# Kernel tuning notes

Hardware: AMD Instinct MI355X
Metric: run time of the kernel (lower is better)

Reference implementation:

```python
import jax, jax.numpy as jnp
import numpy as np

T, HID, H, KV, D = 2048, 2048, 16, 8, 128
EPS = 1e-6
THETA = 10000.0


def setup_inputs() -> dict:
    key = jax.random.key(0)
    ks = jax.random.split(key, 4)
    return {
        "positions": jnp.arange(T, dtype=jnp.int32),
        "hidden_states": jax.random.normal(ks[0], (T, HID), dtype=jnp.float32),
        "layernorm_weight": jnp.ones((HID,), dtype=jnp.float32),
        "qkv_weight": jax.random.normal(ks[1], ((H + 2 * KV) * D, HID), dtype=jnp.float32) * 0.02,
        "q_norm_weight": jnp.ones((D,), dtype=jnp.float32),
        "k_norm_weight": jnp.ones((D,), dtype=jnp.float32),
        "o_weight": jax.random.normal(ks[2], (HID, H * D), dtype=jnp.float32) * 0.02,
    }


def _rms(x, w, eps=EPS):
    var = jnp.mean(jnp.square(x), axis=-1, keepdims=True)
    return x * jax.lax.rsqrt(var + eps) * w


def _rope(x, pos):
    # NeoX-style rotary over full head_dim. x: [T, nH, D]
    inv_freq = 1.0 / (THETA ** (jnp.arange(0, D, 2, dtype=jnp.float32) / D))
    ang = pos.astype(jnp.float32)[:, None] * inv_freq  # [T, D/2]
    cos, sin = jnp.cos(ang)[:, None, :], jnp.sin(ang)[:, None, :]
    x1, x2 = x[..., : D // 2], x[..., D // 2 :]
    return jnp.concatenate([x1 * cos - x2 * sin, x2 * cos + x1 * sin], axis=-1)


def reference(positions, hidden_states, layernorm_weight, qkv_weight,
              q_norm_weight, k_norm_weight, o_weight):
    # Fused RMSNorm + QKV projection
    normed = _rms(hidden_states, layernorm_weight)                 # [T, HID]
    qkv = normed @ qkv_weight.T                                    # [T, (H+2KV)*D]
    q, k, v = jnp.split(qkv, [H * D, (H + KV) * D], axis=-1)
    q = _rms(q.reshape(T, H, D), q_norm_weight)                    # per-head q norm
    k = _rms(k.reshape(T, KV, D), k_norm_weight)                   # per-head k norm
    v = v.reshape(T, KV, D)
    # RoPE
    q = _rope(q, positions)
    k = _rope(k, positions)
    # GQA causal attention
    scale = D ** -0.5
    kr = jnp.repeat(k, H // KV, axis=1)                            # [T, H, D]
    vr = jnp.repeat(v, H // KV, axis=1)
    scores = jnp.einsum("qhd,khd->hqk", q, kr) * scale             # [H, T, T]
    mask = jnp.tril(jnp.ones((T, T), dtype=bool))
    scores = jnp.where(mask[None], scores, jnp.finfo(scores.dtype).min)
    attn = jax.nn.softmax(scores, axis=-1)
    out = jnp.einsum("hqk,khd->qhd", attn, vr).reshape(T, H * D)
    return out @ o_weight.T                                        # [T, HID]
```

## Files before the change

### kernel.cpp

```cpp
#include <hip/hip_runtime.h>
#include <cstdint>
#include <cstddef>

typedef __bf16 bf16;
typedef __attribute__((ext_vector_type(8))) __bf16 bf16x8;
typedef __attribute__((ext_vector_type(4))) float f32x4;

#define T_N   2048
#define HID_N 2048
#define NH    16
#define NKV   8
#define HD    128

#define MFMA(a, b, c) __builtin_amdgcn_mfma_f32_16x16x32_bf16((a), (b), (c), 0, 0, 0)

__device__ __forceinline__ void gl_lds16(const void* g, void* l) {
    __builtin_amdgcn_global_load_lds(
        (const __attribute__((address_space(1))) unsigned int*)g,
        (__attribute__((address_space(3))) unsigned int*)l,
        16, 0, 0);
}

__device__ __forceinline__ uint32_t pk2(float a, float b) {
    union { bf16 h; unsigned short u; } ca, cb;
    ca.h = (bf16)a; cb.h = (bf16)b;
    return ((uint32_t)cb.u << 16) | ca.u;
}

__global__ __launch_bounds__(256) void k_f2b(const float* __restrict__ in,
                                             bf16* __restrict__ out, int n) {
    int i = (blockIdx.x * 256 + threadIdx.x) * 8;
    if (i >= n) return;
    const float4* p = (const float4*)(in + i);
    float4 a = p[0], b = p[1];
    bf16x8 v;
    v[0] = (bf16)a.x; v[1] = (bf16)a.y; v[2] = (bf16)a.z; v[3] = (bf16)a.w;
    v[4] = (bf16)b.x; v[5] = (bf16)b.y; v[6] = (bf16)b.z; v[7] = (bf16)b.w;
    *(bf16x8*)(out + i) = v;
}

__global__ __launch_bounds__(256) void k_rmsnorm(const float* __restrict__ x,
                                                 const float* __restrict__ w,
                                                 bf16* __restrict__ out) {
    int row = blockIdx.x, tid = threadIdx.x;
    const float* xr = x + (size_t)row * HID_N;
    float4 a = ((const float4*)xr)[tid * 2];
    float4 b = ((const float4*)xr)[tid * 2 + 1];
    float ss = a.x*a.x + a.y*a.y + a.z*a.z + a.w*a.w
             + b.x*b.x + b.y*b.y + b.z*b.z + b.w*b.w;
    #pragma unroll
    for (int m = 32; m; m >>= 1) ss += __shfl_xor(ss, m);
    __shared__ float red[4];
    if ((tid & 63) == 0) red[tid >> 6] = ss;
    __syncthreads();
    float tot = red[0] + red[1] + red[2] + red[3];
    float rs = rsqrtf(tot * (1.0f / HID_N) + 1e-6f);
    const float4* wr = (const float4*)(w + tid * 8);
    float4 wa = wr[0], wb = wr[1];
    bf16x8 v;
    v[0] = (bf16)(a.x * rs * wa.x); v[1] = (bf16)(a.y * rs * wa.y);
    v[2] = (bf16)(a.z * rs * wa.z); v[3] = (bf16)(a.w * rs * wa.w);
    v[4] = (bf16)(b.x * rs * wb.x); v[5] = (bf16)(b.y * rs * wb.y);
    v[6] = (bf16)(b.z * rs * wb.z); v[7] = (bf16)(b.w * rs * wb.w);
    *(bf16x8*)(out + (size_t)row * HID_N + tid * 8) = v;
}

__global__ __launch_bounds__(256, 2) void k_gemm_bt(const bf16* __restrict__ A,
                                                    const bf16* __restrict__ B,
                                                    float* __restrict__ C,
                                                    int M, int N, int K) {
    __shared__ __attribute__((aligned(16))) bf16 As[128 * 64];
    __shared__ __attribute__((aligned(16))) bf16 Bs[128 * 64];
    const int tid = threadIdx.x;
    const int lane = tid & 63, wid = tid >> 6;
    const int wm = wid >> 1, wn = wid & 1;
    const int r = lane & 15, g = lane >> 4;
    const size_t bm = (size_t)blockIdx.y * 128, bn = (size_t)blockIdx.x * 128;

    f32x4 acc[4][4] = {};

    const int srow = tid >> 3;
    const int schk = tid & 7;

    for (int k0 = 0; k0 < K; k0 += 64) {
        __syncthreads();
        #pragma unroll
        for (int c = 0; c < 4; c++) {
            int row = c * 32 + srow;
            int ka = (schk ^ (row & 7)) << 3;
            gl_lds16(A + (bm + row) * (size_t)K + k0 + ka,
                     (char*)As + c * 4096 + tid * 16);
            gl_lds16(B + (bn + row) * (size_t)K + k0 + ka,
                     (char*)Bs + c * 4096 + tid * 16);
        }
        __syncthreads();
        #pragma unroll
        for (int kk = 0; kk < 2; kk++) {
            bf16x8 af[4], bfr[4];
            #pragma unroll
            for (int m = 0; m < 4; m++) {
                int row = wm * 64 + m * 16 + r;
                af[m] = *(const bf16x8*)(As + row * 64 + (((kk * 4 + g) ^ (row & 7)) << 3));
            }
            #pragma unroll
            for (int n = 0; n < 4; n++) {
                int row = wn * 64 + n * 16 + r;
                bfr[n] = *(const bf16x8*)(Bs + row * 64 + (((kk * 4 + g) ^ (row & 7)) << 3));
            }
            #pragma unroll
            for (int m = 0; m < 4; m++)
                #pragma unroll
                for (int n = 0; n < 4; n++)
                    acc[m][n] = MFMA(af[m], bfr[n], acc[m][n]);
        }
    }
    #pragma unroll
    for (int m = 0; m < 4; m++)
        #pragma unroll
        for (int n = 0; n < 4; n++)
            #pragma unroll
            for (int j = 0; j < 4; j++) {
                size_t row = bm + wm * 64 + m * 16 + g * 4 + j;
                size_t col = bn + wn * 64 + n * 16 + r;
                C[row * (size_t)N + col] = acc[m][n][j];
            }
}

__global__ __launch_bounds__(128) void k_normrope(const float* __restrict__ qkv,
                                                  const float* __restrict__ qw,
                                                  const float* __restrict__ kw,
                                                  const int* __restrict__ pos,
                                                  bf16* __restrict__ q,
                                                  bf16* __restrict__ k,
                                                  bf16* __restrict__ v) {
    int t = blockIdx.x, hs = blockIdx.y, d = threadIdx.x;
    const float* base = qkv + (size_t)t * 4096;
    if (hs >= 24) {
        int hv = hs - 24;
        v[((size_t)t * NKV + hv) * HD + d] = (bf16)base[3072 + hv * 128 + d];
        return;
    }
    bool isq = hs < 16;
    int h = isq ? hs : hs - 16;
    float x = isq ? base[h * 128 + d] : base[2048 + h * 128 + d];
    float ss = x * x;
    #pragma unroll
    for (int m = 32; m; m >>= 1) ss += __shfl_xor(ss, m);
    __shared__ float red[2];
    if ((d & 63) == 0) red[d >> 6] = ss;
    __syncthreads();
    float rs = rsqrtf((red[0] + red[1]) * (1.0f / HD) + 1e-6f);
    float nx = x * rs * (isq ? qw[d] : kw[d]);
    __shared__ float sh[128];
    sh[d] = nx;
    __syncthreads();
    float other = sh[d ^ 64];
    int j = d & 63;
    float ang = (float)pos[t] * __powf(10000.f, -(float)j * (1.f / 64.f));
    float s, c;
    __sincosf(ang, &s, &c);
    float o = (d < 64) ? (nx * c - other * s) : (nx * c + other * s);
    bf16* dst = isq ? (q + ((size_t)t * NH + h) * HD + d)
                    : (k + ((size_t)t * NKV + h) * HD + d);
    *dst = (bf16)o;
}

__global__ __launch_bounds__(256, 2) void k_flash(const bf16* __restrict__ Q,
                                                  const bf16* __restrict__ K,
                                                  const bf16* __restrict__ V,
                                                  bf16* __restrict__ O) {
    __shared__ __attribute__((aligned(16))) bf16 Ks[64 * 128];
    __shared__ __attribute__((aligned(16))) bf16 Vt[128 * 64];
    const int tid = threadIdx.x, lane = tid & 63, w = tid >> 6;
    const int r = lane & 15, g = lane >> 4;
    const int h = blockIdx.x, by = blockIdx.y;
    const int qt = (by < 16) ? (2 * by) : (63 - 2 * by);
    const int q0 = qt * 64;
    const int gh = h >> 1;
    const int q0w = q0 + w * 16;

    bf16x8 qf[4];
    #pragma unroll
    for (int ks = 0; ks < 4; ks++)
        qf[ks] = *(const bf16x8*)(Q + ((size_t)(q0w + r) * NH + h) * HD + ks * 32 + g * 8);

    f32x4 o_acc[8] = {};
    float m_run = -1e30f, l_run = 0.f;

    const int rowk = tid >> 4, posc = tid & 15;
    const int vd = tid & 127, vhalf = tid >> 7;

    const float scale = 0.08838834764831845f;

    for (int kv0 = 0; kv0 < q0 + 64; kv0 += 64) {
        __syncthreads();
        #pragma unroll
        for (int c = 0; c < 4; c++) {
            int row = c * 16 + rowk;
            int srcc = posc ^ (row & 7);
            gl_lds16(K + ((size_t)(kv0 + row) * NKV + gh) * HD + srcc * 8,
                     (char*)Ks + c * 4096 + tid * 16);
        }
        #pragma unroll
        for (int it = 0; it < 4; it++) {
            int kb = vhalf + it * 2;
            const bf16* src = V + ((size_t)(kv0 + kb * 8) * NKV + gh) * HD + vd;
            bf16x8 col;
            #pragma unroll
            for (int i = 0; i < 8; i++) col[i] = src[(size_t)i * (NKV * HD)];
            *(bf16x8*)(Vt + vd * 64 + ((kb ^ (vd & 7)) * 8)) = col;
        }
        __syncthreads();

        if (kv0 <= q0w + 15) {
            float s[4][4];
            #pragma unroll
            for (int t = 0; t < 4; t++) {
                f32x4 S = {};
                #pragma unroll
                for (int ks = 0; ks < 4; ks++) {
                    int row = t * 16 + r;
                    bf16x8 kf = *(const bf16x8*)(Ks + row * 128 + (((4 * ks + g) ^ (row & 7)) * 8));
                    S = MFMA(kf, qf[ks], S);
                }
                #pragma unroll
                for (int j = 0; j < 4; j++) {
                    int kg = kv0 + t * 16 + 4 * g + j;
                    s[t][j] = (kg <= q0w + r) ? S[j] * scale : -1e30f;
                }
            }
            float mx = s[0][0];
            #pragma unroll
            for (int t = 0; t < 4; t++)
                #pragma unroll
                for (int j = 0; j < 4; j++) mx = fmaxf(mx, s[t][j]);
            mx = fmaxf(mx, __shfl_xor(mx, 16));
            mx = fmaxf(mx, __shfl_xor(mx, 32));
            float mn = fmaxf(m_run, mx);
            float alpha = __expf(m_run - mn);
            m_run = mn;
            float rs = 0.f;
            #pragma unroll
            for (int t = 0; t < 4; t++)
                #pragma unroll
                for (int j = 0; j < 4; j++) {
                    s[t][j] = __expf(s[t][j] - mn);
                    rs += s[t][j];
                }
            rs += __shfl_xor(rs, 16);
            rs += __shfl_xor(rs, 32);
            l_run = l_run * alpha + rs;

            float aO[4];
            #pragma unroll
            for (int j = 0; j < 4; j++) aO[j] = __shfl(alpha, 4 * g + j);
            #pragma unroll
            for (int f = 0; f < 8; f++)
                #pragma unroll
                for (int j = 0; j < 4; j++) o_acc[f][j] *= aO[j];

            uint32_t w0[4], w1[4];
            #pragma unroll
            for (int t = 0; t < 4; t++) {
                w0[t] = pk2(s[t][0], s[t][1]);
                w1[t] = pk2(s[t][2], s[t][3]);
            }
            const int idx0 = (32 * (g & 1) + r) << 2;
            const int idx1 = idx0 + 64;
            const bool hi = (g >> 1) != 0;
            bf16x8 pa[2];
            #pragma unroll
            for (int kk = 0; kk < 2; kk++) {
                int t0 = 2 * kk, t1 = 2 * kk + 1;
                uint32_t a0 = (uint32_t)__builtin_amdgcn_ds_bpermute(idx0, (int)w0[t0]);
                uint32_t b0 = (uint32_t)__builtin_amdgcn_ds_bpermute(idx0, (int)w0[t1]);
                uint32_t a1 = (uint32_t)__builtin_amdgcn_ds_bpermute(idx0, (int)w1[t0]);
                uint32_t b1 = (uint32_t)__builtin_amdgcn_ds_bpermute(idx0, (int)w1[t1]);
                uint32_t a2 = (uint32_t)__builtin_amdgcn_ds_bpermute(idx1, (int)w0[t0]);
                uint32_t b2 = (uint32_t)__builtin_amdgcn_ds_bpermute(idx1, (int)w0[t1]);
                uint32_t a3 = (uint32_t)__builtin_amdgcn_ds_bpermute(idx1, (int)w1[t0]);
                uint32_t b3 = (uint32_t)__builtin_amdgcn_ds_bpermute(idx1, (int)w1[t1]);
                union { uint32_t u[4]; bf16x8 v; } P;
                P.u[0] = hi ? b0 : a0;
                P.u[1] = hi ? b1 : a1;
                P.u[2] = hi ? b2 : a2;
                P.u[3] = hi ? b3 : a3;
                pa[kk] = P.v;
            }

            #pragma unroll
            for (int f = 0; f < 8; f++) {
                int d = f * 16 + r;
                #pragma unroll
                for (int kk = 0; kk < 2; kk++) {
                    bf16x8 vf = *(const bf16x8*)(Vt + d * 64 + (((4 * kk + g) ^ (d & 7)) * 8));
                    o_acc[f] = MFMA(pa[kk], vf, o_acc[f]);
                }
            }
        }
    }
    float lO[4];
    #pragma unroll
    for (int j = 0; j < 4; j++) lO[j] = __shfl(l_run, 4 * g + j);
    #pragma unroll
    for (int f = 0; f < 8; f++)
        #pragma unroll
        for (int j = 0; j < 4; j++) {
            int qq = q0w + 4 * g + j;
            int d = f * 16 + r;
            O[((size_t)qq * NH + h) * HD + d] = (bf16)(o_acc[f][j] / lO[j]);
        }
}

extern "C" void kernel_launch(void* const* d_in, const int* in_sizes, int n_in,
                              void* d_out, int out_size, void* d_ws, size_t ws_size,
                              hipStream_t stream) {
    const int*   pos  = (const int*)d_in[0];
    const float* hid  = (const float*)d_in[1];
    const float* lw   = (const float*)d_in[2];
    const float* qkvw = (const float*)d_in[3];
    const float* qnw  = (const float*)d_in[4];
    const float* knw  = (const float*)d_in[5];
    const float* ow   = (const float*)d_in[6];
    float* out = (float*)d_out;

    char* ws = (char*)d_ws;
    bf16*  qkvw_b = (bf16*)(ws);
    bf16*  ow_b   = (bf16*)(ws + (16u << 20));
    bf16*  normed = (bf16*)(ws + (24u << 20));
    float* qkvf   = (float*)(ws + (32u << 20));
    bf16*  qb     = (bf16*)(ws + (64u << 20));
    bf16*  kb     = (bf16*)(ws + (72u << 20));
    bf16*  vb     = (bf16*)(ws + (76u << 20));
    bf16*  ao     = normed;

    k_f2b<<<4096, 256, 0, stream>>>(qkvw, qkvw_b, 4096 * 2048);
    k_f2b<<<2048, 256, 0, stream>>>(ow, ow_b, 2048 * 2048);
    k_rmsnorm<<<T_N, 256, 0, stream>>>(hid, lw, normed);
    k_gemm_bt<<<dim3(32, 16), 256, 0, stream>>>(normed, qkvw_b, qkvf, 2048, 4096, 2048);
    k_normrope<<<dim3(T_N, 32), 128, 0, stream>>>(qkvf, qnw, knw, pos, qb, kb, vb);
    k_flash<<<dim3(NH, 32), 256, 0, stream>>>(qb, kb, vb, ao);
    k_gemm_bt<<<dim3(16, 16), 256, 0, stream>>>(ao, ow_b, out, 2048, 2048, 2048);
}
```

Measured before the change: 205.6 us.

## Double-buffer K/V in flash attention and compute transposed PV without lane permutes

The attention kernel now keeps two LDS buffers for K and V. It prefetches the next tile, K through global-to-LDS loads and V through registers, while the current tile is computed, so there is one barrier per iteration instead of two. The P·V product is rewritten as Vᵀ·Pᵀ using 16x16x16 bf16 MFMAs. Because the score fragment already sits in the right lane layout, the ds_bpermute shuffles and the alpha/l broadcasts go away, and the output is written as 4-wide vector stores. It also adds s_setprio around the MFMA sections and drops the per-wave causal skip, so fully masked tiles are now computed. LDS use per block doubles, which may limit occupancy.

Measured after the change: 196.8 us. -4.3%, faster.

```diff
diff --git a/kernel.cpp b/kernel.cpp
--- a/kernel.cpp
+++ b/kernel.cpp
@@ -4,7 +4,9 @@
 
 typedef __bf16 bf16;
 typedef __attribute__((ext_vector_type(8))) __bf16 bf16x8;
+typedef __attribute__((ext_vector_type(4))) __bf16 bf16x4v;
 typedef __attribute__((ext_vector_type(4))) float f32x4;
+typedef __attribute__((ext_vector_type(4))) short short4v;
 
 #define T_N   2048
 #define HID_N 2048
@@ -13,6 +15,16 @@
 #define HD    128
 
 #define MFMA(a, b, c) __builtin_amdgcn_mfma_f32_16x16x32_bf16((a), (b), (c), 0, 0, 0)
+
+__device__ __forceinline__ f32x4 MFMA16(short4v a, short4v b, f32x4 c) {
+#if __has_builtin(__builtin_amdgcn_mfma_f32_16x16x16bf16_1k)
+    return __builtin_amdgcn_mfma_f32_16x16x16bf16_1k(a, b, c, 0, 0, 0);
+#else
+    asm volatile("v_mfma_f32_16x16x16_bf16 %0, %1, %2, %0\n\ts_nop 7\n\ts_nop 7"
+                 : "+v"(c) : "v"(a), "v"(b));
+    return c;
+#endif
+}
 
 __device__ __forceinline__ void gl_lds16(const void* g, void* l) {
     __builtin_amdgcn_global_load_lds(
@@ -169,8 +181,9 @@
                                                   const bf16* __restrict__ K,
                                                   const bf16* __restrict__ V,
                                                   bf16* __restrict__ O) {
-    __shared__ __attribute__((aligned(16))) bf16 Ks[64 * 128];
-    __shared__ __attribute__((aligned(16))) bf16 Vt[128 * 64];
+    __shared__ __attribute__((aligned(16))) bf16 Ks2[2][64 * 128];
+    __shared__ __attribute__((aligned(16))) bf16 Vt2[2][128 * 64];
+
     const int tid = threadIdx.x, lane = tid & 63, w = tid >> 6;
     const int r = lane & 15, g = lane >> 4;
     const int h = blockIdx.x, by = blockIdx.y;
@@ -179,137 +192,147 @@
     const int gh = h >> 1;
     const int q0w = q0 + w * 16;
 
+    const int rowk = tid >> 4, posc = tid & 15;
+    const int vd = tid & 127, vhalf = tid >> 7;
+
     bf16x8 qf[4];
     #pragma unroll
     for (int ks = 0; ks < 4; ks++)
         qf[ks] = *(const bf16x8*)(Q + ((size_t)(q0w + r) * NH + h) * HD + ks * 32 + g * 8);
 
-    f32x4 o_acc[8] = {};
+    f32x4 acc[8] = {};
     float m_run = -1e30f, l_run = 0.f;
-
-    const int rowk = tid >> 4, posc = tid & 15;
-    const int vd = tid & 127, vhalf = tid >> 7;
-
     const float scale = 0.08838834764831845f;
-
-    for (int kv0 = 0; kv0 < q0 + 64; kv0 += 64) {
-        __syncthreads();
+    const int nt = qt + 1;
+
+    {
         #pragma unroll
         for (int c = 0; c < 4; c++) {
             int row = c * 16 + rowk;
             int srcc = posc ^ (row & 7);
-            gl_lds16(K + ((size_t)(kv0 + row) * NKV + gh) * HD + srcc * 8,
-                     (char*)Ks + c * 4096 + tid * 16);
-        }
+            gl_lds16(K + ((size_t)row * NKV + gh) * HD + srcc * 8,
+                     (char*)&Ks2[0][0] + c * 4096 + tid * 16);
+        }
+        bf16x8 vr[4];
         #pragma unroll
         for (int it = 0; it < 4; it++) {
             int kb = vhalf + it * 2;
-            const bf16* src = V + ((size_t)(kv0 + kb * 8) * NKV + gh) * HD + vd;
-            bf16x8 col;
-            #pragma unroll
-            for (int i = 0; i < 8; i++) col[i] = src[(size_t)i * (NKV * HD)];
-            *(bf16x8*)(Vt + vd * 64 + ((kb ^ (vd & 7)) * 8)) = col;
+            const bf16* src = V + ((size_t)(kb * 8) * NKV + gh) * HD + vd;
+            #pragma unroll
+            for (int i = 0; i < 8; i++) vr[it][i] = src[(size_t)i * (NKV * HD)];
+        }
+        #pragma unroll
+        for (int it = 0; it < 4; it++) {
+            int kb = vhalf + it * 2;
+            *(bf16x8*)(&Vt2[0][0] + vd * 64 + ((kb ^ (vd & 7)) * 8)) = vr[it];
         }
         __syncthreads();
-
-        if (kv0 <= q0w + 15) {
-            float s[4][4];
-            #pragma unroll
-            for (int t = 0; t < 4; t++) {
+    }
+
+    for (int t = 0; t < nt; ++t) {
+        const int b = t & 1;
+        const int kv0 = t * 64;
+        const bool pf = (t + 1 < nt);
+        bf16x8 vr[4];
+        if (pf) {
+            const int kv1 = kv0 + 64;
+            #pragma unroll
+            for (int c = 0; c < 4; c++) {
+                int row = c * 16 + rowk;
+                int srcc = posc ^ (row & 7);
+                gl_lds16(K + ((size_t)(kv1 + row) * NKV + gh) * HD + srcc * 8,
+                         (char*)&Ks2[0][0] + (b ^ 1) * 16384 + c * 4096 + tid * 16);
+            }
+            #pragma unroll
+            for (int it = 0; it < 4; it++) {
+                int kb = vhalf + it * 2;
+                const bf16* src = V + ((size_t)(kv1 + kb * 8) * NKV + gh) * HD + vd;
+                #pragma unroll
+                for (int i = 0; i < 8; i++) vr[it][i] = src[(size_t)i * (NKV * HD)];
+            }
+        }
+        {
+            const bf16* Kb = &Ks2[b][0];
+            const char* Vb = (const char*)&Vt2[b][0];
+            float sc[4][4];
+            __builtin_amdgcn_s_setprio(1);
+            #pragma unroll
+            for (int t4 = 0; t4 < 4; t4++) {
                 f32x4 S = {};
                 #pragma unroll
                 for (int ks = 0; ks < 4; ks++) {
-                    int row = t * 16 + r;
-                    bf16x8 kf = *(const bf16x8*)(Ks + row * 128 + (((4 * ks + g) ^ (row & 7)) * 8));
+                    int row = t4 * 16 + r;
+                    bf16x8 kf = *(const bf16x8*)(Kb + row * 128 + (((4 * ks + g) ^ (row & 7)) * 8));
                     S = MFMA(kf, qf[ks], S);
                 }
                 #pragma unroll
                 for (int j = 0; j < 4; j++) {
-                    int kg = kv0 + t * 16 + 4 * g + j;
-                    s[t][j] = (kg <= q0w + r) ? S[j] * scale : -1e30f;
+                    int kg = kv0 + t4 * 16 + 4 * g + j;
+                    sc[t4][j] = (kg <= q0w + r) ? S[j] * scale : -1e30f;
                 }
             }
-            float mx = s[0][0];
-            #pragma unroll
-            for (int t = 0; t < 4; t++)
-                #pragma unroll
-                for (int j = 0; j < 4; j++) mx = fmaxf(mx, s[t][j]);
+            __builtin_amdgcn_s_setprio(0);
+            float mx = sc[0][0];
+            #pragma unroll
+            for (int t4 = 0; t4 < 4; t4++)
+                #pragma unroll
+                for (int j = 0; j < 4; j++) mx = fmaxf(mx, sc[t4][j]);
             mx = fmaxf(mx, __shfl_xor(mx, 16));
             mx = fmaxf(mx, __shfl_xor(mx, 32));
             float mn = fmaxf(m_run, mx);
             float alpha = __expf(m_run - mn);
             m_run = mn;
-            float rs = 0.f;
-            #pragma unroll
-            for (int t = 0; t < 4; t++)
+            float rsum = 0.f;
+            #pragma unroll
+            for (int t4 = 0; t4 < 4; t4++)
                 #pragma unroll
                 for (int j = 0; j < 4; j++) {
-                    s[t][j] = __expf(s[t][j] - mn);
-                    rs += s[t][j];
+                    sc[t4][j] = __expf(sc[t4][j] - mn);
+                    rsum += sc[t4][j];
                 }
-            rs += __shfl_xor(rs, 16);
-            rs += __shfl_xor(rs, 32);
-            l_run = l_run * alpha + rs;
-
-            float aO[4];
-            #pragma unroll
-            for (int j = 0; j < 4; j++) aO[j] = __shfl(alpha, 4 * g + j);
+            rsum += __shfl_xor(rsum, 16);
+            rsum += __shfl_xor(rsum, 32);
+            l_run = l_run * alpha + rsum;
             #pragma unroll
             for (int f = 0; f < 8; f++)
                 #pragma unroll
-                for (int j = 0; j < 4; j++) o_acc[f][j] *= aO[j];
-
-            uint32_t w0[4], w1[4];
-            #pragma unroll
-            for (int t = 0; t < 4; t++) {
-                w0[t] = pk2(s[t][0], s[t][1]);
-                w1[t] = pk2(s[t][2], s[t][3]);
-            }
-            const int idx0 = (32 * (g & 1) + r) << 2;
-            const int idx1 = idx0 + 64;
-            const bool hi = (g >> 1) != 0;
-            bf16x8 pa[2];
-            #pragma unroll
-            for (int kk = 0; kk < 2; kk++) {
-                int t0 = 2 * kk, t1 = 2 * kk + 1;
-                uint32_t a0 = (uint32_t)__builtin_amdgcn_ds_bpermute(idx0, (int)w0[t0]);
-                uint32_t b0 = (uint32_t)__builtin_amdgcn_ds_bpermute(idx0, (int)w0[t1]);
-                uint32_t a1 = (uint32_t)__builtin_amdgcn_ds_bpermute(idx0, (int)w1[t0]);
-                uint32_t b1 = (uint32_t)__builtin_amdgcn_ds_bpermute(idx0, (int)w1[t1]);
-                uint32_t a2 = (uint32_t)__builtin_amdgcn_ds_bpermute(idx1, (int)w0[t0]);
-                uint32_t b2 = (uint32_t)__builtin_amdgcn_ds_bpermute(idx1, (int)w0[t1]);
-                uint32_t a3 = (uint32_t)__builtin_amdgcn_ds_bpermute(idx1, (int)w1[t0]);
-                uint32_t b3 = (uint32_t)__builtin_amdgcn_ds_bpermute(idx1, (int)w1[t1]);
-                union { uint32_t u[4]; bf16x8 v; } P;
-                P.u[0] = hi ? b0 : a0;
-                P.u[1] = hi ? b1 : a1;
-                P.u[2] = hi ? b2 : a2;
-                P.u[3] = hi ? b3 : a3;
-                pa[kk] = P.v;
-            }
-
+                for (int j = 0; j < 4; j++) acc[f][j] *= alpha;
+            union PB { uint32_t u[2]; short4v s; };
+            PB pbu[4];
+            #pragma unroll
+            for (int t4 = 0; t4 < 4; t4++) {
+                pbu[t4].u[0] = pk2(sc[t4][0], sc[t4][1]);
+                pbu[t4].u[1] = pk2(sc[t4][2], sc[t4][3]);
+            }
+            __builtin_amdgcn_s_setprio(1);
             #pragma unroll
             for (int f = 0; f < 8; f++) {
-                int d = f * 16 + r;
-                #pragma unroll
-                for (int kk = 0; kk < 2; kk++) {
-                    bf16x8 vf = *(const bf16x8*)(Vt + d * 64 + (((4 * kk + g) ^ (d & 7)) * 8));
-                    o_acc[f] = MFMA(pa[kk], vf, o_acc[f]);
+                #pragma unroll
+                for (int t4 = 0; t4 < 4; t4++) {
+                    short4v vf = *(const short4v*)(Vb + f * 2048 + r * 128 +
+                                  (((2 * t4 + (g >> 1)) ^ (r & 7)) * 16) + (g & 1) * 8);
+                    acc[f] = MFMA16(vf, pbu[t4].s, acc[f]);
                 }
             }
-        }
-    }
-    float lO[4];
-    #pragma unroll
-    for (int j = 0; j < 4; j++) lO[j] = __shfl(l_run, 4 * g + j);
-    #pragma unroll
-    for (int f = 0; f < 8; f++)
-        #pragma unroll
-        for (int j = 0; j < 4; j++) {
-            int qq = q0w + 4 * g + j;
-            int d = f * 16 + r;
-            O[((size_t)qq * NH + h) * HD + d] = (bf16)(o_acc[f][j] / lO[j]);
-        }
+            __builtin_amdgcn_s_setprio(0);
+        }
+        if (pf) {
+            #pragma unroll
+            for (int it = 0; it < 4; it++) {
+                int kb = vhalf + it * 2;
+                *(bf16x8*)(&Vt2[0][0] + (b ^ 1) * 8192 + vd * 64 + ((kb ^ (vd & 7)) * 8)) = vr[it];
+            }
+        }
+        __syncthreads();
+    }
+    float inv_l = 1.0f / l_run;
+    #pragma unroll
+    for (int f = 0; f < 8; f++) {
+        bf16x4v ov;
+        #pragma unroll
+        for (int j = 0; j < 4; j++) ov[j] = (bf16)(acc[f][j] * inv_l);
+        *(bf16x4v*)(O + ((size_t)(q0w + r) * NH + h) * HD + f * 16 + 4 * g) = ov;
+    }
 }
 
 extern "C" void kernel_launch(void* const* d_in, const int* in_sizes, int n_in,
```
